# Kernel tuning notes

Measured on AMD Instinct MI355X. Metric: run time of the kernel, lower is better.

## Reference

```python
import jax, jax.numpy as jnp
import numpy as np

M, H, D, P = 16, 32, 128, 8192
N = H * D


def setup_inputs() -> dict:
    key = jax.random.key(0)
    k1, k2, k3, k4, k5, k6 = jax.random.split(key, 6)
    X = jax.random.normal(k1, (M, N), dtype=jnp.float32)
    # small init scale keeps the module's naive (unstabilized) exp-softmax finite
    Wq = jax.random.normal(k2, (N, N), dtype=jnp.float32) * 0.02
    Wk = jax.random.normal(k3, (N, N), dtype=jnp.float32) * 0.02
    Wv = jax.random.normal(k4, (N, N), dtype=jnp.float32) * 0.02
    cache_K = jax.random.normal(k5, (H, P, D), dtype=jnp.float32) * 0.05
    cache_V = jax.random.normal(k6, (H, P, D), dtype=jnp.float32)
    return {"X": X, "Wq": Wq, "Wk": Wk, "Wv": Wv,
            "cache_K": cache_K, "cache_V": cache_V}


def reference(X, Wq, Wk, Wv, cache_K, cache_V):
    m, n = X.shape                      # [M, N]
    h, p, d = cache_K.shape             # [H, P, D]
    # RMSNorm (no learned scale, matches (X*X).sum / N)
    x2 = jnp.sum(X * X, axis=1)
    x_norm = X / jnp.sqrt(x2 / n)[:, None]
    # QKV projections (nn.Linear, no bias -> x @ W.T)
    q = (x_norm @ Wq.T).reshape(m, h, d).transpose(1, 0, 2)   # [H, M, D]
    k = (x_norm @ Wk.T).reshape(m, h, d).transpose(1, 0, 2)   # [H, M, D]
    v = (x_norm @ Wv.T).reshape(m, h, d).transpose(1, 0, 2)   # [H, M, D]
    # append to cache
    ck = jnp.concatenate([cache_K, k], axis=1)                # [H, P+M, D]
    cv = jnp.concatenate([cache_V, v], axis=1)                # [H, P+M, D]
    # scores (no 1/sqrt(D) scaling in the original) + naive softmax
    c = jnp.einsum('hmd,hpd->hmp', q, ck)                     # [H, M, P+M]
    c_exp = jnp.exp(c)
    c_div = c_exp / jnp.sum(c_exp, axis=2, keepdims=True)
    o = jnp.einsum('hmp,hpd->hmd', c_div, cv)                 # [H, M, D]
    return o.transpose(1, 0, 2).reshape(m, n)                 # [M, N]
```

## Files before the change

kernel.cpp:

```cpp
#include <hip/hip_runtime.h>

#define NN 4096
#define HH 32
#define DD 128
#define MM 16
#define PP 8192

__device__ __forceinline__ float dot4f(float4 a, float4 b) {
  return a.x * b.x + a.y * b.y + a.z * b.z + a.w * b.w;
}

__global__ void k1_rms(const float* __restrict__ X, float* __restrict__ inv) {
  const int m = blockIdx.x;
  const int tid = threadIdx.x;
  float s = 0.f;
#pragma unroll
  for (int i = 0; i < 16; ++i) {
    float v = X[(size_t)m * NN + i * 256 + tid];
    s += v * v;
  }
#pragma unroll
  for (int off = 1; off < 64; off <<= 1) s += __shfl_xor(s, off, 64);
  __shared__ float red[4];
  if ((tid & 63) == 0) red[tid >> 6] = s;
  __syncthreads();
  if (tid == 0) {
    float t = red[0] + red[1] + red[2] + red[3];
    inv[m] = rsqrtf(t * (1.0f / (float)NN));
  }
}

__global__ __launch_bounds__(256, 4) void k2_qkv(
    const float* __restrict__ X, const float* __restrict__ Wq,
    const float* __restrict__ Wk, const float* __restrict__ Wv,
    float* __restrict__ c_part) {
  __shared__ float lds_c[4][64][18];
  const int b = blockIdx.x;
  const int mat = b >> 8;
  const int rem = b & 255;
  const int qt = rem >> 6;
  const int jg = rem & 63;
  const float* W = (mat == 0) ? Wq : (mat == 1) ? Wk : Wv;
  const int tid = threadIdx.x;
  const int wave = tid >> 6;
  const int lane = tid & 63;
  const int m4 = lane & 3;
  const int g = lane >> 2;
  const int kbase = qt * 1024 + wave * 256 + g * 16;

  float4 xr[4][4];
#pragma unroll
  for (int mi = 0; mi < 4; ++mi) {
    const float* xp = X + (size_t)(mi * 4 + m4) * NN + kbase;
#pragma unroll
    for (int j = 0; j < 4; ++j) xr[mi][j] = *(const float4*)(xp + j * 4);
  }

  const int j0 = jg * 64;
  for (int grp = 0; grp < 16; ++grp) {
    float acc[4][4];
#pragma unroll
    for (int r = 0; r < 4; ++r)
#pragma unroll
      for (int mi = 0; mi < 4; ++mi) acc[r][mi] = 0.f;
#pragma unroll
    for (int r = 0; r < 4; ++r) {
      const float* wp = W + (size_t)(j0 + grp * 4 + r) * NN + kbase;
      float4 w0 = *(const float4*)(wp);
      float4 w1 = *(const float4*)(wp + 4);
      float4 w2 = *(const float4*)(wp + 8);
      float4 w3 = *(const float4*)(wp + 12);
#pragma unroll
      for (int mi = 0; mi < 4; ++mi)
        acc[r][mi] = acc[r][mi] + dot4f(xr[mi][0], w0) + dot4f(xr[mi][1], w1) +
                     dot4f(xr[mi][2], w2) + dot4f(xr[mi][3], w3);
    }
#pragma unroll
    for (int off = 4; off < 64; off <<= 1)
#pragma unroll
      for (int r = 0; r < 4; ++r)
#pragma unroll
        for (int mi = 0; mi < 4; ++mi)
          acc[r][mi] += __shfl_xor(acc[r][mi], off, 64);
    if (g == 0) {
#pragma unroll
      for (int r = 0; r < 4; ++r)
#pragma unroll
        for (int mi = 0; mi < 4; ++mi)
          lds_c[wave][grp * 4 + r][mi * 4 + m4] = acc[r][mi];
    }
  }
  __syncthreads();
#pragma unroll
  for (int i = 0; i < 4; ++i) {
    const int m = i * 4 + (tid >> 6);
    const int j = tid & 63;
    float s = lds_c[0][j][m] + lds_c[1][j][m] + lds_c[2][j][m] + lds_c[3][j][m];
    c_part[(((size_t)(mat * 4 + qt) * 16 + m) << 12) + (j0 + j)] = s;
  }
}

__global__ void k2b_combine(const float* __restrict__ c_part,
                            const float* __restrict__ inv,
                            float* __restrict__ qkv) {
  const int t = blockIdx.x * 256 + threadIdx.x;
  const int mat = t >> 16;
  const int r = t & 65535;
  const int h = r >> 11;
  const int m = (r >> 7) & 15;
  const int d = r & 127;
  const int j = h * 128 + d;
  float s = 0.f;
#pragma unroll
  for (int qt = 0; qt < 4; ++qt)
    s += c_part[(((size_t)(mat * 4 + qt) * 16 + m) << 12) + j];
  qkv[t] = s * inv[m];
}

__global__ __launch_bounds__(256, 4) void k3_attn(
    const float* __restrict__ cK, const float* __restrict__ cV,
    const float* __restrict__ qkv, float* __restrict__ o_part,
    float* __restrict__ denom_part) {
  __shared__ float smem[8192];
  __shared__ float dlds[4][16];
  const int chunk = blockIdx.x;
  const int h = blockIdx.y;
  const int tid = threadIdx.x;
  const int wave = tid >> 6;
  const int lane = tid & 63;
  const int m4 = lane & 3;
  const int g = lane >> 2;
  const int d0 = g * 8;

  float4 qr[4][2];
  {
    const float* qf = qkv + (size_t)h * 2048;
#pragma unroll
    for (int mi = 0; mi < 4; ++mi) {
      const float* qp = qf + (mi * 4 + m4) * 128 + d0;
      qr[mi][0] = *(const float4*)(qp);
      qr[mi][1] = *(const float4*)(qp + 4);
    }
  }
  float oacc[4][8];
#pragma unroll
  for (int mi = 0; mi < 4; ++mi)
#pragma unroll
    for (int j = 0; j < 8; ++j) oacc[mi][j] = 0.f;
  float den[4] = {0.f, 0.f, 0.f, 0.f};

  const float* Ksrc;
  const float* Vsrc;
  int np;
  if (chunk < 32) {
    Ksrc = cK + ((size_t)h * PP + chunk * 256) * DD;
    Vsrc = cV + ((size_t)h * PP + chunk * 256) * DD;
    np = 256;
  } else {
    Ksrc = qkv + 65536 + (size_t)h * 2048;
    Vsrc = qkv + 131072 + (size_t)h * 2048;
    np = 16;
  }

  for (int t0 = 0; t0 < np; t0 += 32) {
    const int rows = (np - t0 < 32) ? (np - t0) : 32;
    const int nf4 = rows * 32;
    const float4* gk = (const float4*)(Ksrc + (size_t)t0 * DD);
    const float4* gv = (const float4*)(Vsrc + (size_t)t0 * DD);
    for (int s = tid; s < nf4; s += 256) {
      ((float4*)smem)[s] = gk[s];
      ((float4*)(smem + 4096))[s] = gv[s];
    }
    __syncthreads();
    const int per = rows >> 2;
#pragma unroll 4
    for (int pi = 0; pi < per; ++pi) {
      const int p = wave * per + pi;
      const float* kp = smem + p * DD + d0;
      float4 ka = *(const float4*)(kp);
      float4 kb = *(const float4*)(kp + 4);
      float c[4];
#pragma unroll
      for (int mi = 0; mi < 4; ++mi)
        c[mi] = dot4f(qr[mi][0], ka) + dot4f(qr[mi][1], kb);
#pragma unroll
      for (int off = 4; off < 64; off <<= 1)
#pragma unroll
        for (int mi = 0; mi < 4; ++mi) c[mi] += __shfl_xor(c[mi], off, 64);
      const float* vp = smem + 4096 + p * DD + d0;
      float4 va = *(const float4*)(vp);
      float4 vb = *(const float4*)(vp + 4);
#pragma unroll
      for (int mi = 0; mi < 4; ++mi) {
        float e = __expf(c[mi]);
        den[mi] += e;
        oacc[mi][0] += e * va.x;
        oacc[mi][1] += e * va.y;
        oacc[mi][2] += e * va.z;
        oacc[mi][3] += e * va.w;
        oacc[mi][4] += e * vb.x;
        oacc[mi][5] += e * vb.y;
        oacc[mi][6] += e * vb.z;
        oacc[mi][7] += e * vb.w;
      }
    }
    __syncthreads();
  }
#pragma unroll
  for (int mi = 0; mi < 4; ++mi) {
    float* op = smem + wave * 2048 + (mi * 4 + m4) * 128 + d0;
    *(float4*)(op) = make_float4(oacc[mi][0], oacc[mi][1], oacc[mi][2], oacc[mi][3]);
    *(float4*)(op + 4) = make_float4(oacc[mi][4], oacc[mi][5], oacc[mi][6], oacc[mi][7]);
  }
  if (g == 0) {
#pragma unroll
    for (int mi = 0; mi < 4; ++mi) dlds[wave][mi * 4 + m4] = den[mi];
  }
  __syncthreads();
  const size_t ob = ((size_t)h * 33 + chunk) * 2048;
#pragma unroll
  for (int i = 0; i < 8; ++i) {
    const int md = i * 256 + tid;
    o_part[ob + md] = smem[md] + smem[2048 + md] + smem[4096 + md] + smem[6144 + md];
  }
  if (tid < 16)
    denom_part[((size_t)h * 33 + chunk) * 16 + tid] =
        dlds[0][tid] + dlds[1][tid] + dlds[2][tid] + dlds[3][tid];
}

__global__ void k4_final(const float* __restrict__ o_part,
                         const float* __restrict__ denom_part,
                         float* __restrict__ out) {
  const int h = blockIdx.x;
  const int tid = threadIdx.x;
  __shared__ float dinv[16];
  if (tid < 16) {
    float s = 0.f;
    for (int c = 0; c < 33; ++c) s += denom_part[((size_t)h * 33 + c) * 16 + tid];
    dinv[tid] = 1.0f / s;
  }
  __syncthreads();
#pragma unroll
  for (int i = 0; i < 8; ++i) {
    const int md = i * 256 + tid;
    float s = 0.f;
    for (int c = 0; c < 33; ++c) s += o_part[((size_t)h * 33 + c) * 2048 + md];
    const int m = md >> 7;
    const int d = md & 127;
    out[(size_t)m * NN + h * DD + d] = s * dinv[m];
  }
}

extern "C" void kernel_launch(void* const* d_in, const int* in_sizes, int n_in,
                              void* d_out, int out_size, void* d_ws, size_t ws_size,
                              hipStream_t stream) {
  (void)in_sizes; (void)n_in; (void)out_size; (void)ws_size;
  const float* X  = (const float*)d_in[0];
  const float* Wq = (const float*)d_in[1];
  const float* Wk = (const float*)d_in[2];
  const float* Wv = (const float*)d_in[3];
  const float* cK = (const float*)d_in[4];
  const float* cV = (const float*)d_in[5];
  float* out = (float*)d_out;
  float* ws = (float*)d_ws;

  float* inv        = ws;
  float* c_part     = ws + 16;
  float* qkv        = c_part + 786432;
  float* o_part     = qkv + 196608;
  float* denom_part = o_part + 2162688;

  k1_rms<<<16, 256, 0, stream>>>(X, inv);
  k2_qkv<<<768, 256, 0, stream>>>(X, Wq, Wk, Wv, c_part);
  k2b_combine<<<768, 256, 0, stream>>>(c_part, inv, qkv);
  k3_attn<<<dim3(33, 32), 256, 0, stream>>>(cK, cV, qkv, o_part, denom_part);
  k4_final<<<32, 256, 0, stream>>>(o_part, denom_part, out);
}
```

Baseline: 502.8 us.

## Fuse QKV combine into attention, drop LDS staging, widen grids

```diff
diff --git a/kernel.cpp b/kernel.cpp
--- a/kernel.cpp
+++ b/kernel.cpp
@@ -6,8 +6,16 @@
 #define MM 16
 #define PP 8192
 
+__device__ __forceinline__ float4 ld4(const float* p) { return *(const float4*)p; }
 __device__ __forceinline__ float dot4f(float4 a, float4 b) {
   return a.x * b.x + a.y * b.y + a.z * b.z + a.w * b.w;
+}
+__device__ __forceinline__ void accumv(float* o, float e, float4 a, float4 b,
+                                       float4 c, float4 d) {
+  o[0] += e * a.x;  o[1] += e * a.y;  o[2] += e * a.z;  o[3] += e * a.w;
+  o[4] += e * b.x;  o[5] += e * b.y;  o[6] += e * b.z;  o[7] += e * b.w;
+  o[8] += e * c.x;  o[9] += e * c.y;  o[10] += e * c.z; o[11] += e * c.w;
+  o[12] += e * d.x; o[13] += e * d.y; o[14] += e * d.z; o[15] += e * d.w;
 }
 
 __global__ void k1_rms(const float* __restrict__ X, float* __restrict__ inv) {
@@ -34,12 +42,12 @@
     const float* __restrict__ X, const float* __restrict__ Wq,
     const float* __restrict__ Wk, const float* __restrict__ Wv,
     float* __restrict__ c_part) {
-  __shared__ float lds_c[4][64][18];
+  __shared__ float lds_c[4][32][18];
   const int b = blockIdx.x;
-  const int mat = b >> 8;
-  const int rem = b & 255;
-  const int qt = rem >> 6;
-  const int jg = rem & 63;
+  const int mat = b >> 9;
+  const int rem = b & 511;
+  const int qt = rem >> 7;
+  const int jg = rem & 127;
   const float* W = (mat == 0) ? Wq : (mat == 1) ? Wk : Wv;
   const int tid = threadIdx.x;
   const int wave = tid >> 6;
@@ -53,11 +61,11 @@
   for (int mi = 0; mi < 4; ++mi) {
     const float* xp = X + (size_t)(mi * 4 + m4) * NN + kbase;
 #pragma unroll
-    for (int j = 0; j < 4; ++j) xr[mi][j] = *(const float4*)(xp + j * 4);
-  }
-
-  const int j0 = jg * 64;
-  for (int grp = 0; grp < 16; ++grp) {
+    for (int j = 0; j < 4; ++j) xr[mi][j] = ld4(xp + j * 4);
+  }
+
+  const int j0 = jg * 32;
+  for (int grp = 0; grp < 8; ++grp) {
     float acc[4][4];
 #pragma unroll
     for (int r = 0; r < 4; ++r)
@@ -66,10 +74,10 @@
 #pragma unroll
     for (int r = 0; r < 4; ++r) {
       const float* wp = W + (size_t)(j0 + grp * 4 + r) * NN + kbase;
-      float4 w0 = *(const float4*)(wp);
-      float4 w1 = *(const float4*)(wp + 4);
-      float4 w2 = *(const float4*)(wp + 8);
-      float4 w3 = *(const float4*)(wp + 12);
+      float4 w0 = ld4(wp);
+      float4 w1 = ld4(wp + 4);
+      float4 w2 = ld4(wp + 8);
+      float4 w3 = ld4(wp + 12);
 #pragma unroll
       for (int mi = 0; mi < 4; ++mi)
         acc[r][mi] = acc[r][mi] + dot4f(xr[mi][0], w0) + dot4f(xr[mi][1], w1) +
@@ -92,163 +100,172 @@
   }
   __syncthreads();
 #pragma unroll
-  for (int i = 0; i < 4; ++i) {
-    const int m = i * 4 + (tid >> 6);
-    const int j = tid & 63;
+  for (int i = 0; i < 2; ++i) {
+    const int idx = i * 256 + tid;
+    const int j = idx & 31;
+    const int m = idx >> 5;
     float s = lds_c[0][j][m] + lds_c[1][j][m] + lds_c[2][j][m] + lds_c[3][j][m];
     c_part[(((size_t)(mat * 4 + qt) * 16 + m) << 12) + (j0 + j)] = s;
   }
 }
 
-__global__ void k2b_combine(const float* __restrict__ c_part,
-                            const float* __restrict__ inv,
-                            float* __restrict__ qkv) {
-  const int t = blockIdx.x * 256 + threadIdx.x;
-  const int mat = t >> 16;
-  const int r = t & 65535;
-  const int h = r >> 11;
-  const int m = (r >> 7) & 15;
-  const int d = r & 127;
-  const int j = h * 128 + d;
-  float s = 0.f;
-#pragma unroll
-  for (int qt = 0; qt < 4; ++qt)
-    s += c_part[(((size_t)(mat * 4 + qt) * 16 + m) << 12) + j];
-  qkv[t] = s * inv[m];
-}
-
 __global__ __launch_bounds__(256, 4) void k3_attn(
     const float* __restrict__ cK, const float* __restrict__ cV,
-    const float* __restrict__ qkv, float* __restrict__ o_part,
-    float* __restrict__ denom_part) {
-  __shared__ float smem[8192];
-  __shared__ float dlds[4][16];
+    const float* __restrict__ c_part, const float* __restrict__ inv,
+    float* __restrict__ o_part, float* __restrict__ denom_part) {
   const int chunk = blockIdx.x;
   const int h = blockIdx.y;
   const int tid = threadIdx.x;
   const int wave = tid >> 6;
   const int lane = tid & 63;
-  const int m4 = lane & 3;
-  const int g = lane >> 2;
-  const int d0 = g * 8;
-
-  float4 qr[4][2];
+  const int m8 = lane & 7;
+  const int g = lane >> 3;
+  const int d0 = g * 16;
+
+  float4 qa[4], qb[4];
   {
-    const float* qf = qkv + (size_t)h * 2048;
-#pragma unroll
-    for (int mi = 0; mi < 4; ++mi) {
-      const float* qp = qf + (mi * 4 + m4) * 128 + d0;
-      qr[mi][0] = *(const float4*)(qp);
-      qr[mi][1] = *(const float4*)(qp + 4);
-    }
-  }
-  float oacc[4][8];
-#pragma unroll
-  for (int mi = 0; mi < 4; ++mi)
-#pragma unroll
-    for (int j = 0; j < 8; ++j) oacc[mi][j] = 0.f;
-  float den[4] = {0.f, 0.f, 0.f, 0.f};
-
-  const float* Ksrc;
-  const float* Vsrc;
-  int np;
+    float f[2][16];
+#pragma unroll
+    for (int mi = 0; mi < 2; ++mi)
+#pragma unroll
+      for (int j = 0; j < 16; ++j) f[mi][j] = 0.f;
+#pragma unroll
+    for (int qt = 0; qt < 4; ++qt) {
+#pragma unroll
+      for (int mi = 0; mi < 2; ++mi) {
+        const int m = mi * 8 + m8;
+        const float* cp = c_part + (((size_t)(qt * 16 + m)) << 12) + h * DD + d0;
+#pragma unroll
+        for (int j = 0; j < 4; ++j) {
+          float4 t = ld4(cp + j * 4);
+          f[mi][j * 4 + 0] += t.x;
+          f[mi][j * 4 + 1] += t.y;
+          f[mi][j * 4 + 2] += t.z;
+          f[mi][j * 4 + 3] += t.w;
+        }
+      }
+    }
+    const float i0 = inv[m8];
+    const float i1 = inv[8 + m8];
+#pragma unroll
+    for (int j = 0; j < 4; ++j) {
+      qa[j] = make_float4(f[0][j * 4] * i0, f[0][j * 4 + 1] * i0,
+                          f[0][j * 4 + 2] * i0, f[0][j * 4 + 3] * i0);
+      qb[j] = make_float4(f[1][j * 4] * i1, f[1][j * 4 + 1] * i1,
+                          f[1][j * 4 + 2] * i1, f[1][j * 4 + 3] * i1);
+    }
+  }
+
+  float oac0[16], oac1[16];
+#pragma unroll
+  for (int j = 0; j < 16; ++j) { oac0[j] = 0.f; oac1[j] = 0.f; }
+  float den0 = 0.f, den1 = 0.f;
+
   if (chunk < 32) {
-    Ksrc = cK + ((size_t)h * PP + chunk * 256) * DD;
-    Vsrc = cV + ((size_t)h * PP + chunk * 256) * DD;
-    np = 256;
+    const size_t rowb = ((size_t)h * PP + chunk * 256 + wave * 64) * DD;
+    const float* kb = cK + rowb + d0;
+    const float* vb = cV + rowb + d0;
+#pragma unroll 2
+    for (int pi = 0; pi < 64; ++pi) {
+      const float* kp = kb + pi * DD;
+      float4 k0 = ld4(kp), k1 = ld4(kp + 4), k2 = ld4(kp + 8), k3 = ld4(kp + 12);
+      const float* vp = vb + pi * DD;
+      float4 v0 = ld4(vp), v1 = ld4(vp + 4), v2 = ld4(vp + 8), v3 = ld4(vp + 12);
+      float c0 = dot4f(qa[0], k0) + dot4f(qa[1], k1) + dot4f(qa[2], k2) + dot4f(qa[3], k3);
+      float c1 = dot4f(qb[0], k0) + dot4f(qb[1], k1) + dot4f(qb[2], k2) + dot4f(qb[3], k3);
+#pragma unroll
+      for (int off = 8; off < 64; off <<= 1) {
+        c0 += __shfl_xor(c0, off, 64);
+        c1 += __shfl_xor(c1, off, 64);
+      }
+      float e0 = __expf(c0), e1 = __expf(c1);
+      den0 += e0; den1 += e1;
+      accumv(oac0, e0, v0, v1, v2, v3);
+      accumv(oac1, e1, v0, v1, v2, v3);
+    }
   } else {
-    Ksrc = qkv + 65536 + (size_t)h * 2048;
-    Vsrc = qkv + 131072 + (size_t)h * 2048;
-    np = 16;
-  }
-
-  for (int t0 = 0; t0 < np; t0 += 32) {
-    const int rows = (np - t0 < 32) ? (np - t0) : 32;
-    const int nf4 = rows * 32;
-    const float4* gk = (const float4*)(Ksrc + (size_t)t0 * DD);
-    const float4* gv = (const float4*)(Vsrc + (size_t)t0 * DD);
-    for (int s = tid; s < nf4; s += 256) {
-      ((float4*)smem)[s] = gk[s];
-      ((float4*)(smem + 4096))[s] = gv[s];
-    }
-    __syncthreads();
-    const int per = rows >> 2;
-#pragma unroll 4
-    for (int pi = 0; pi < per; ++pi) {
-      const int p = wave * per + pi;
-      const float* kp = smem + p * DD + d0;
-      float4 ka = *(const float4*)(kp);
-      float4 kb = *(const float4*)(kp + 4);
-      float c[4];
-#pragma unroll
-      for (int mi = 0; mi < 4; ++mi)
-        c[mi] = dot4f(qr[mi][0], ka) + dot4f(qr[mi][1], kb);
-#pragma unroll
-      for (int off = 4; off < 64; off <<= 1)
-#pragma unroll
-        for (int mi = 0; mi < 4; ++mi) c[mi] += __shfl_xor(c[mi], off, 64);
-      const float* vp = smem + 4096 + p * DD + d0;
-      float4 va = *(const float4*)(vp);
-      float4 vb = *(const float4*)(vp + 4);
-#pragma unroll
-      for (int mi = 0; mi < 4; ++mi) {
-        float e = __expf(c[mi]);
-        den[mi] += e;
-        oacc[mi][0] += e * va.x;
-        oacc[mi][1] += e * va.y;
-        oacc[mi][2] += e * va.z;
-        oacc[mi][3] += e * va.w;
-        oacc[mi][4] += e * vb.x;
-        oacc[mi][5] += e * vb.y;
-        oacc[mi][6] += e * vb.z;
-        oacc[mi][7] += e * vb.w;
-      }
-    }
-    __syncthreads();
-  }
-#pragma unroll
-  for (int mi = 0; mi < 4; ++mi) {
-    float* op = smem + wave * 2048 + (mi * 4 + m4) * 128 + d0;
-    *(float4*)(op) = make_float4(oacc[mi][0], oacc[mi][1], oacc[mi][2], oacc[mi][3]);
-    *(float4*)(op + 4) = make_float4(oacc[mi][4], oacc[mi][5], oacc[mi][6], oacc[mi][7]);
+#pragma unroll
+    for (int pi = 0; pi < 4; ++pi) {
+      const int p = wave * 4 + pi;
+      float kk[16], vv[16];
+#pragma unroll
+      for (int j = 0; j < 16; ++j) { kk[j] = 0.f; vv[j] = 0.f; }
+#pragma unroll
+      for (int qt = 0; qt < 4; ++qt) {
+        const float* cpk = c_part + (((size_t)((4 + qt) * 16 + p)) << 12) + h * DD + d0;
+        const float* cpv = c_part + (((size_t)((8 + qt) * 16 + p)) << 12) + h * DD + d0;
+#pragma unroll
+        for (int j = 0; j < 4; ++j) {
+          float4 tk = ld4(cpk + j * 4);
+          float4 tv = ld4(cpv + j * 4);
+          kk[j * 4 + 0] += tk.x; kk[j * 4 + 1] += tk.y;
+          kk[j * 4 + 2] += tk.z; kk[j * 4 + 3] += tk.w;
+          vv[j * 4 + 0] += tv.x; vv[j * 4 + 1] += tv.y;
+          vv[j * 4 + 2] += tv.z; vv[j * 4 + 3] += tv.w;
+        }
+      }
+      const float ip = inv[p];
+      float4 k0 = make_float4(kk[0] * ip, kk[1] * ip, kk[2] * ip, kk[3] * ip);
+      float4 k1 = make_float4(kk[4] * ip, kk[5] * ip, kk[6] * ip, kk[7] * ip);
+      float4 k2 = make_float4(kk[8] * ip, kk[9] * ip, kk[10] * ip, kk[11] * ip);
+      float4 k3 = make_float4(kk[12] * ip, kk[13] * ip, kk[14] * ip, kk[15] * ip);
+      float4 v0 = make_float4(vv[0] * ip, vv[1] * ip, vv[2] * ip, vv[3] * ip);
+      float4 v1 = make_float4(vv[4] * ip, vv[5] * ip, vv[6] * ip, vv[7] * ip);
+      float4 v2 = make_float4(vv[8] * ip, vv[9] * ip, vv[10] * ip, vv[11] * ip);
+      float4 v3 = make_float4(vv[12] * ip, vv[13] * ip, vv[14] * ip, vv[15] * ip);
+      float c0 = dot4f(qa[0], k0) + dot4f(qa[1], k1) + dot4f(qa[2], k2) + dot4f(qa[3], k3);
+      float c1 = dot4f(qb[0], k0) + dot4f(qb[1], k1) + dot4f(qb[2], k2) + dot4f(qb[3], k3);
+#pragma unroll
+      for (int off = 8; off < 64; off <<= 1) {
+        c0 += __shfl_xor(c0, off, 64);
+        c1 += __shfl_xor(c1, off, 64);
+      }
+      float e0 = __expf(c0), e1 = __expf(c1);
+      den0 += e0; den1 += e1;
+      accumv(oac0, e0, v0, v1, v2, v3);
+      accumv(oac1, e1, v0, v1, v2, v3);
+    }
+  }
+
+  const size_t wc = ((size_t)h * 33 + chunk) * 4 + wave;
+  float* op0 = o_part + wc * 2048 + m8 * DD + d0;
+  float* op1 = o_part + wc * 2048 + (8 + m8) * DD + d0;
+#pragma unroll
+  for (int j = 0; j < 4; ++j) {
+    *(float4*)(op0 + j * 4) = make_float4(oac0[j * 4], oac0[j * 4 + 1],
+                                          oac0[j * 4 + 2], oac0[j * 4 + 3]);
+    *(float4*)(op1 + j * 4) = make_float4(oac1[j * 4], oac1[j * 4 + 1],
+                                          oac1[j * 4 + 2], oac1[j * 4 + 3]);
   }
   if (g == 0) {
-#pragma unroll
-    for (int mi = 0; mi < 4; ++mi) dlds[wave][mi * 4 + m4] = den[mi];
-  }
-  __syncthreads();
-  const size_t ob = ((size_t)h * 33 + chunk) * 2048;
-#pragma unroll
-  for (int i = 0; i < 8; ++i) {
-    const int md = i * 256 + tid;
-    o_part[ob + md] = smem[md] + smem[2048 + md] + smem[4096 + md] + smem[6144 + md];
-  }
-  if (tid < 16)
-    denom_part[((size_t)h * 33 + chunk) * 16 + tid] =
-        dlds[0][tid] + dlds[1][tid] + dlds[2][tid] + dlds[3][tid];
+    denom_part[wc * 16 + m8] = den0;
+    denom_part[wc * 16 + 8 + m8] = den1;
+  }
 }
 
 __global__ void k4_final(const float* __restrict__ o_part,
                          const float* __restrict__ denom_part,
                          float* __restrict__ out) {
-  const int h = blockIdx.x;
-  const int tid = threadIdx.x;
-  __shared__ float dinv[16];
-  if (tid < 16) {
+  const int b = blockIdx.x;
+  const int h = b >> 3;
+  const int sub = b & 7;
+  const int tid = threadIdx.x;
+  const int md = sub * 256 + tid;
+  __shared__ float dinv[2];
+  if (tid == 0 || tid == 128) {
+    const int mm = md >> 7;
     float s = 0.f;
-    for (int c = 0; c < 33; ++c) s += denom_part[((size_t)h * 33 + c) * 16 + tid];
-    dinv[tid] = 1.0f / s;
+    for (int c = 0; c < 132; ++c)
+      s += denom_part[((size_t)h * 132 + c) * 16 + mm];
+    dinv[tid >> 7] = 1.0f / s;
   }
   __syncthreads();
-#pragma unroll
-  for (int i = 0; i < 8; ++i) {
-    const int md = i * 256 + tid;
-    float s = 0.f;
-    for (int c = 0; c < 33; ++c) s += o_part[((size_t)h * 33 + c) * 2048 + md];
-    const int m = md >> 7;
-    const int d = md & 127;
-    out[(size_t)m * NN + h * DD + d] = s * dinv[m];
-  }
+  float s = 0.f;
+  for (int c = 0; c < 132; ++c)
+    s += o_part[((size_t)h * 132 + c) * 2048 + md];
+  const int m = md >> 7;
+  const int d = md & 127;
+  out[(size_t)m * NN + h * DD + d] = s * dinv[tid >> 7];
 }
 
 extern "C" void kernel_launch(void* const* d_in, const int* in_sizes, int n_in,
@@ -266,13 +283,11 @@
 
   float* inv        = ws;
   float* c_part     = ws + 16;
-  float* qkv        = c_part + 786432;
-  float* o_part     = qkv + 196608;
-  float* denom_part = o_part + 2162688;
+  float* o_part     = c_part + 786432;
+  float* denom_part = o_part + 8650752;
 
   k1_rms<<<16, 256, 0, stream>>>(X, inv);
-  k2_qkv<<<768, 256, 0, stream>>>(X, Wq, Wk, Wv, c_part);
-  k2b_combine<<<768, 256, 0, stream>>>(c_part, inv, qkv);
-  k3_attn<<<dim3(33, 32), 256, 0, stream>>>(cK, cV, qkv, o_part, denom_part);
-  k4_final<<<32, 256, 0, stream>>>(o_part, denom_part, out);
-}
+  k2_qkv<<<1536, 256, 0, stream>>>(X, Wq, Wk, Wv, c_part);
+  k3_attn<<<dim3(33, 32), 256, 0, stream>>>(cK, cV, c_part, inv, o_part, denom_part);
+  k4_final<<<256, 256, 0, stream>>>(o_part, denom_part, out);
+}
```

New measurement: 537.1 us. 6.8% more time.
